# Kernel optimization log

Measured on AMD Instinct MI355X. Metric: run time of the kernel, lower is better.

Reference implementation:

```python
import jax, jax.numpy as jnp
import numpy as np

N_ITER = 2          # GenSP n_iter
M_COEF = 0.0        # GenSP M (grid strength)
AFF_SOFTMAX = 1.0   # GenSP affinity_softmax
NEG_INF = -1e30


def setup_inputs() -> dict:
    key = jax.random.key(0)
    x = jax.random.normal(key, (4, 64, 256, 256), dtype=jnp.float32)
    return {"x": x, "stoken": 16}


def _candidates(H, W, sh, sw, nH, nW):
    # 3x3 neighborhood of each pixel's initial superpixel (SSN / get_abs_indices)
    bi = jnp.arange(H) // sh
    bj = jnp.arange(W) // sw
    di = jnp.repeat(jnp.array([-1, 0, 1]), 3)   # (9,)
    dj = jnp.tile(jnp.array([-1, 0, 1]), 3)     # (9,)
    ci = bi[:, None, None] + di                 # (H,1,9)
    cj = bj[None, :, None] + dj                 # (1,W,9)
    valid = (ci >= 0) & (ci < nH) & (cj >= 0) & (cj < nW)        # (H,W,9)
    cand = jnp.clip(ci, 0, nH - 1) * nW + jnp.clip(cj, 0, nW - 1)  # (H,W,9)
    cand = jnp.broadcast_to(cand, (H, W, 9)).reshape(H * W, 9)
    valid = jnp.broadcast_to(valid, (H, W, 9)).reshape(H * W, 9)
    return cand, valid


def _affinity(feats, cent, cand, valid, nS):
    # feats: (B,Cf,P)  cent: (B,Cf,nS)  cand/valid: (P,9)
    B, Cf, P = feats.shape
    dot = jnp.einsum('bcp,bcs->bps', feats, cent)            # (B,P,nS) GEMM
    f2 = jnp.sum(feats * feats, axis=1)                      # (B,P)
    c2 = jnp.sum(cent * cent, axis=1)                        # (B,nS)
    dot9 = jnp.take_along_axis(dot, cand[None], axis=2)      # (B,P,9)
    dist = f2[..., None] + c2[:, cand] - 2.0 * dot9          # l2 distance (B,P,9)
    logits = jnp.where(valid[None], -AFF_SOFTMAX * dist, NEG_INF)
    aff9 = jax.nn.softmax(logits, axis=-1)                   # softmax_order 'v0'
    aff9 = jnp.where(valid[None], aff9, 0.0)
    # dense scatter: A[b, cand[p,k], p] += aff9[b,p,k]  -> (B,nS,P)
    pidx = jnp.arange(P)[:, None]
    A = jnp.zeros((B, nS, P), feats.dtype).at[:, cand, pidx].add(aff9)
    return A


def reference(x, stoken):
    B, C, H, W = x.shape
    sh = sw = int(stoken)
    nH, nW = (H - 1) // sh + 1, (W - 1) // sw + 1
    nS, P = nH * nW, H * W
    # append_grid: concat scaled pixel-coordinate channels (M / stoken)
    gi, gj = jnp.meshgrid(jnp.arange(H, dtype=x.dtype), jnp.arange(W, dtype=x.dtype), indexing='ij')
    grid = jnp.broadcast_to((M_COEF / sh) * jnp.stack([gi, gj]), (B, 2, H, W))
    feats = jnp.concatenate([x, grid], axis=1)               # (B,C+2,H,W)
    Cf = C + 2
    # init centroids: adaptive_avg_pool2d == block mean (H,W divisible by stoken)
    cent = feats.reshape(B, Cf, nH, sh, nW, sw).mean(axis=(3, 5)).reshape(B, Cf, nS)
    feats = feats.reshape(B, Cf, P)
    cand, valid = _candidates(H, W, sh, sw, nH, nW)
    A = None
    for k in range(N_ITER):
        A = _affinity(feats, cent, cand, valid, nS)          # (B,nS,P)
        if k < N_ITER - 1:
            num = jnp.einsum('bsp,bcp->bcs', A, feats)       # (B,Cf,nS)
            den = jnp.sum(A, axis=2)[:, None, :] + 1e-16
            cent = num / den
    return A
```

## Files before the change

kernel.cpp:

```cpp
#include <hip/hip_runtime.h>


#define PP 65536

typedef __attribute__((ext_vector_type(8))) short short8;
typedef __attribute__((ext_vector_type(4))) float f32x4;

__device__ __forceinline__ unsigned short f2bf(float f) {
  unsigned u = __float_as_uint(f);
  u += 0x7fff + ((u >> 16) & 1);
  return (unsigned short)(u >> 16);
}

__global__ __launch_bounds__(256) void k_init(const float* __restrict__ x,
                                              float* __restrict__ cent0,
                                              float4* __restrict__ zero4) {
  __shared__ float blk[64];
  int t = threadIdx.x;
  int wg = blockIdx.x;
  int cg = wg & 15, bi = (wg >> 4) & 15, b = wg >> 8;
  int tid = wg * 256 + t;
  if (tid < 16640) zero4[tid] = make_float4(0.f, 0.f, 0.f, 0.f);
  if (t < 64) blk[t] = 0.f;
  __syncthreads();
  int sub = t >> 6, j4 = t & 63;
#pragma unroll
  for (int q = 0; q < 4; q++) {
    int c = cg * 4 + q;
    const float4* xp4 =
        (const float4*)(x + ((long)(b * 64 + c) << 16) + ((bi * 16 + sub * 4) << 8)) + j4;
    float4 a = make_float4(0.f, 0.f, 0.f, 0.f);
#pragma unroll
    for (int r = 0; r < 4; r++) {
      float4 v = xp4[r * 64];
      a.x += v.x; a.y += v.y; a.z += v.z; a.w += v.w;
    }
    float ps = a.x + a.y + a.z + a.w;
    ps += __shfl_xor(ps, 1);
    ps += __shfl_xor(ps, 2);
    if ((j4 & 3) == 0) atomicAdd(&blk[(j4 >> 2) * 4 + q], ps);
  }
  __syncthreads();
  if (t < 64) {
    int sj = t >> 2, q = t & 3;
    cent0[(((b << 8) + bi * 16 + sj) << 6) + cg * 4 + q] = blk[t] * (1.f / 256.f);
  }
}

__global__ __launch_bounds__(256) void k_stat(const float* __restrict__ x,
                                              const float* __restrict__ cent,
                                              float* __restrict__ num,
                                              float* __restrict__ den) {
  __shared__ __align__(16) unsigned short xbf[64 * 264];
  __shared__ __align__(16) unsigned short affbf[16 * 264];
  __shared__ float cent_s[9 * 64];
  __shared__ float c2p[72];
  __shared__ float c2_s[9];
  __shared__ float den_s[36];
  __shared__ int scand[9];

  int t = threadIdx.x;
  int wg = blockIdx.x;
  int bj = wg & 15, bi = (wg >> 4) & 15, b = wg >> 8;

  if (t < 9) {
    int di = t / 3 - 1, dj = t % 3 - 1;
    int ci = bi + di, cj = bj + dj;
    int sc = min(max(ci, 0), 15) * 16 + min(max(cj, 0), 15);
    bool valid = ((unsigned)ci < 16u) && ((unsigned)cj < 16u);
    scand[t] = valid ? sc : (-1 - sc);
  }
  for (int o = t; o < 144; o += 256) {
    int k = o >> 4, f4 = o & 15;
    int di = k / 3 - 1, dj = k % 3 - 1;
    int sc = min(max(bi + di, 0), 15) * 16 + min(max(bj + dj, 0), 15);
    *(float4*)&cent_s[k * 64 + f4 * 4] =
        *(const float4*)(cent + (((b << 8) + sc) << 6) + f4 * 4);
  }
  __syncthreads();
  if (t < 72) {
    int k = t >> 3, pt = t & 7;
    float s = 0.f;
#pragma unroll
    for (int m = 0; m < 8; m++) { float v = cent_s[k * 64 + pt * 8 + m]; s += v * v; }
    c2p[t] = s;
  }
  __syncthreads();
  if (t < 9) {
    float s = 0.f;
#pragma unroll
    for (int m = 0; m < 8; m++) s += c2p[t * 8 + m];
    c2_s[t] = s;
  }
  __syncthreads();

  int vbits = 0;
#pragma unroll
  for (int k = 0; k < 9; k++) {
    int ci = bi + k / 3 - 1, cj = bj + k % 3 - 1;
    if ((unsigned)ci < 16u && (unsigned)cj < 16u) vbits |= 1 << k;
  }

  int r = t >> 4, col = t & 15;
  const float* base = x + ((long)(b * 64) << 16) + ((bi * 16 + r) << 8) + (bj * 16 + col);
  float acc[9];
#pragma unroll
  for (int k = 0; k < 9; k++) acc[k] = 0.f;
#pragma unroll 8
  for (int c = 0; c < 64; c++) {
    float xv = base[(long)c << 16];
    xbf[c * 264 + t] = f2bf(xv);
#pragma unroll
    for (int k = 0; k < 9; k++) acc[k] = fmaf(xv, cent_s[k * 64 + c], acc[k]);
  }
  float mx = -1e30f;
#pragma unroll
  for (int k = 0; k < 9; k++) {
    float l = 2.f * acc[k] - c2_s[k];
    acc[k] = ((vbits >> k) & 1) ? l : -1e30f;
    mx = fmaxf(mx, acc[k]);
  }
  float sum = 0.f;
#pragma unroll
  for (int k = 0; k < 9; k++) {
    acc[k] = __expf(acc[k] - mx);
    sum += acc[k];
  }
  float rs = 1.f / sum;
#pragma unroll
  for (int k = 0; k < 9; k++) {
    acc[k] *= rs;
    affbf[k * 264 + t] = f2bf(acc[k]);
  }

  int lane = t & 63, w = t >> 6;
#pragma unroll
  for (int k = 0; k < 9; k++) {
    float v = acc[k];
    v += __shfl_xor(v, 1);
    v += __shfl_xor(v, 2);
    v += __shfl_xor(v, 4);
    v += __shfl_xor(v, 8);
    v += __shfl_xor(v, 16);
    v += __shfl_xor(v, 32);
    if (lane == 0) den_s[w * 9 + k] = v;
  }
  __syncthreads();
  if (t < 9) {
    float d = den_s[t] + den_s[9 + t] + den_s[18 + t] + den_s[27 + t];
    int sc = scand[t]; sc = sc >= 0 ? sc : (-1 - sc);
    atomicAdd(&den[(b << 8) + sc], d);
  }

  int mrow = lane & 15;
  int quad = lane >> 4;
  f32x4 dacc = {0.f, 0.f, 0.f, 0.f};
#pragma unroll
  for (int ks = 0; ks < 8; ks++) {
    int p0 = ks * 32 + quad * 8;
    short8 a = *(const short8*)&xbf[(w * 16 + mrow) * 264 + p0];
    short8 bf = *(const short8*)&affbf[mrow * 264 + p0];
    dacc = __builtin_amdgcn_mfma_f32_16x16x32_bf16(a, bf, dacc, 0, 0, 0);
  }
  int kcol = lane & 15;
  if (kcol < 9) {
    int sc = scand[kcol]; sc = sc >= 0 ? sc : (-1 - sc);
    float* np = num + (((b << 8) + sc) << 6) + w * 16 + quad * 4;
    atomicAdd(&np[0], dacc[0]);
    atomicAdd(&np[1], dacc[1]);
    atomicAdd(&np[2], dacc[2]);
    atomicAdd(&np[3], dacc[3]);
  }
}

__global__ __launch_bounds__(256) void k_out(const float* __restrict__ x,
                                             const float* __restrict__ num,
                                             const float* __restrict__ den,
                                             f32x4* __restrict__ out4) {
  __shared__ float cent_s[48 * 68];
  __shared__ float den_s[48];
  __shared__ float c2p[384];
  __shared__ float c2_s[48];
  __shared__ float aff_t[9 * 260];

  int t = threadIdx.x;
  int wg = blockIdx.x;
  int h = wg & 1, i = (wg >> 1) & 255, b = wg >> 9;
  int bi = i >> 4;

  if (t < 48) {
    int ci = min(max(bi - 1 + (t >> 4), 0), 15);
    int cj = t & 15;
    den_s[t] = den[(b << 8) + ci * 16 + cj] + 1e-16f;
  }
  __syncthreads();
  for (int o = t; o < 768; o += 256) {
    int lr = o >> 4, f4i = o & 15;
    int ci = min(max(bi - 1 + (lr >> 4), 0), 15);
    int cj = lr & 15;
    float4 v = *(const float4*)(num + (((b << 8) + ci * 16 + cj) << 6) + f4i * 4);
    float inv = 1.f / den_s[lr];
    v.x *= inv; v.y *= inv; v.z *= inv; v.w *= inv;
    *(float4*)&cent_s[lr * 68 + f4i * 4] = v;
  }
  __syncthreads();
  for (int o = t; o < 384; o += 256) {
    int lr = o >> 3, pt = o & 7;
    float s = 0.f;
#pragma unroll
    for (int m = 0; m < 8; m++) { float v = cent_s[lr * 68 + pt * 8 + m]; s += v * v; }
    c2p[o] = s;
  }
  __syncthreads();
  if (t < 48) {
    float s = 0.f;
#pragma unroll
    for (int m = 0; m < 8; m++) s += c2p[t * 8 + m];
    c2_s[t] = s;
  }
  __syncthreads();

  int j = t, bj = j >> 4;
  int cidx[9];
  float c2k[9];
  int vbits = 0;
#pragma unroll
  for (int k = 0; k < 9; k++) {
    int di = k / 3 - 1, dj = k % 3 - 1;
    int ciu = bi + di, cju = bj + dj;
    if ((unsigned)ciu < 16u && (unsigned)cju < 16u) vbits |= 1 << k;
    int lidx = (di + 1) * 16 + min(max(cju, 0), 15);
    cidx[k] = lidx * 68;
    c2k[k] = c2_s[lidx];
  }
  const float* base = x + ((long)(b * 64) << 16) + (i << 8) + j;
  float acc[9];
#pragma unroll
  for (int k = 0; k < 9; k++) acc[k] = 0.f;
#pragma unroll 8
  for (int c = 0; c < 64; c++) {
    float xv = base[(long)c << 16];
#pragma unroll
    for (int k = 0; k < 9; k++) acc[k] = fmaf(xv, cent_s[cidx[k] + c], acc[k]);
  }
  float mx = -1e30f;
#pragma unroll
  for (int k = 0; k < 9; k++) {
    float l = 2.f * acc[k] - c2k[k];
    acc[k] = ((vbits >> k) & 1) ? l : -1e30f;
    mx = fmaxf(mx, acc[k]);
  }
  float sum = 0.f;
#pragma unroll
  for (int k = 0; k < 9; k++) {
    acc[k] = __expf(acc[k] - mx);
    sum += acc[k];
  }
  float rs = 1.f / sum;
#pragma unroll
  for (int k = 0; k < 9; k++) aff_t[k * 260 + j] = acc[k] * rs;
  __syncthreads();

  f32x4* obase = out4 + ((long)(b << 8) << 14) + (i << 6) + (t & 63);
  int j4 = t & 63;
  int w = t >> 6;
  int s0 = h << 7;
#pragma unroll 4
  for (int m = 0; m < 32; m++) {
    int s = s0 | (m << 2) | w;
    f32x4 v = {0.f, 0.f, 0.f, 0.f};
    int di = (s >> 4) - bi;
    if ((unsigned)(di + 1) <= 2u) {
      int dj = (s & 15) - (j4 >> 2);
      if ((unsigned)(dj + 1) <= 2u) {
        int k = (di + 1) * 3 + dj + 1;
        v = *(const f32x4*)&aff_t[k * 260 + (j4 << 2)];
      }
    }
    __builtin_nontemporal_store(v, &obase[(long)s << 14]);
  }
}

extern "C" void kernel_launch(void* const* d_in, const int* in_sizes, int n_in,
                              void* d_out, int out_size, void* d_ws, size_t ws_size,
                              hipStream_t stream) {
  const float* x = (const float*)d_in[0];
  float* out = (float*)d_out;
  float* ws = (float*)d_ws;

  float* num   = ws;
  float* den   = ws + 65536;
  float* cent0 = ws + 66560;

  k_init<<<1024, 256, 0, stream>>>(x, cent0, (float4*)ws);
  k_stat<<<1024, 256, 0, stream>>>(x, cent0, num, den);
  k_out<<<2048, 256, 0, stream>>>(x, num, den, (f32x4*)out);
}
```

Measured before the change: 353.0 us.

## Split final output stage into centroid, affinity, and dense-write kernels

```diff
diff --git a/kernel.cpp b/kernel.cpp
--- a/kernel.cpp
+++ b/kernel.cpp
@@ -170,6 +170,111 @@
     atomicAdd(&np[1], dacc[1]);
     atomicAdd(&np[2], dacc[2]);
     atomicAdd(&np[3], dacc[3]);
+  }
+}
+
+__global__ __launch_bounds__(256) void k_cent(const float* __restrict__ num,
+                                              const float* __restrict__ den,
+                                              float* __restrict__ cent1,
+                                              float* __restrict__ c2) {
+  int t = threadIdx.x;
+  int idx = blockIdx.x * 4 + (t >> 6);
+  int c = t & 63;
+  float d = den[idx] + 1e-16f;
+  float v = num[(idx << 6) + c] / d;
+  cent1[(idx << 6) + c] = v;
+  float s2 = v * v;
+  s2 += __shfl_xor(s2, 1);
+  s2 += __shfl_xor(s2, 2);
+  s2 += __shfl_xor(s2, 4);
+  s2 += __shfl_xor(s2, 8);
+  s2 += __shfl_xor(s2, 16);
+  s2 += __shfl_xor(s2, 32);
+  if (c == 0) c2[idx] = s2;
+}
+
+__global__ __launch_bounds__(256) void k_aff(const float* __restrict__ x,
+                                             const float* __restrict__ cent,
+                                             const float* __restrict__ c2,
+                                             float* __restrict__ aff) {
+  __shared__ float cent_s[9 * 64];
+  __shared__ float c2_s[9];
+
+  int t = threadIdx.x;
+  int wg = blockIdx.x;
+  int bj = wg & 15, bi = (wg >> 4) & 15, b = wg >> 8;
+
+  for (int o = t; o < 144; o += 256) {
+    int k = o >> 4, f4 = o & 15;
+    int sc = min(max(bi + k / 3 - 1, 0), 15) * 16 + min(max(bj + k % 3 - 1, 0), 15);
+    *(float4*)&cent_s[k * 64 + f4 * 4] =
+        *(const float4*)(cent + (((b << 8) + sc) << 6) + f4 * 4);
+  }
+  if (t < 9) {
+    int sc = min(max(bi + t / 3 - 1, 0), 15) * 16 + min(max(bj + t % 3 - 1, 0), 15);
+    c2_s[t] = c2[(b << 8) + sc];
+  }
+  __syncthreads();
+
+  int vbits = 0;
+#pragma unroll
+  for (int k = 0; k < 9; k++) {
+    int ci = bi + k / 3 - 1, cj = bj + k % 3 - 1;
+    if ((unsigned)ci < 16u && (unsigned)cj < 16u) vbits |= 1 << k;
+  }
+
+  int r = t >> 4, col = t & 15;
+  const float* base = x + ((long)(b * 64) << 16) + ((bi * 16 + r) << 8) + (bj * 16 + col);
+  float acc[9];
+#pragma unroll
+  for (int k = 0; k < 9; k++) acc[k] = 0.f;
+#pragma unroll 8
+  for (int c = 0; c < 64; c++) {
+    float xv = base[(long)c << 16];
+#pragma unroll
+    for (int k = 0; k < 9; k++) acc[k] = fmaf(xv, cent_s[k * 64 + c], acc[k]);
+  }
+  float mx = -1e30f;
+#pragma unroll
+  for (int k = 0; k < 9; k++) {
+    float l = 2.f * acc[k] - c2_s[k];
+    acc[k] = ((vbits >> k) & 1) ? l : -1e30f;
+    mx = fmaxf(mx, acc[k]);
+  }
+  float sum = 0.f;
+#pragma unroll
+  for (int k = 0; k < 9; k++) {
+    acc[k] = __expf(acc[k] - mx);
+    sum += acc[k];
+  }
+  float rs = 1.f / sum;
+  int p = ((bi * 16 + r) << 8) + (bj * 16 + col);
+#pragma unroll
+  for (int k = 0; k < 9; k++)
+    aff[(((long)(b * 9 + k)) << 16) + p] = acc[k] * rs;
+}
+
+__global__ __launch_bounds__(256) void k_write(const float* __restrict__ aff,
+                                               f32x4* __restrict__ out4) {
+  int t = threadIdx.x;
+  int wg = blockIdx.x;
+  int s = wg & 255, b = wg >> 8;
+  int si = s >> 4, sj = s & 15;
+  f32x4* op = out4 + ((long)wg << 14);
+  const f32x4 zero = {0.f, 0.f, 0.f, 0.f};
+#pragma unroll 4
+  for (int m = 0; m < 64; m++) {
+    int idx = m * 256 + t;
+    int i = idx >> 6, j4 = idx & 63;
+    int kr = si - (i >> 4) + 1;
+    int kc = sj - (j4 >> 2) + 1;
+    f32x4 v = zero;
+    if ((unsigned)kr <= 2u && (unsigned)kc <= 2u) {
+      int k = kr * 3 + kc;
+      const f32x4* ap = (const f32x4*)(aff + (((long)(b * 9 + k)) << 16));
+      v = ap[idx];
+    }
+    __builtin_nontemporal_store(v, &op[idx]);
   }
 }
 
@@ -291,8 +396,19 @@
   float* num   = ws;
   float* den   = ws + 65536;
   float* cent0 = ws + 66560;
+  float* cent1 = ws + 132096;
+  float* c2    = ws + 197632;
+  float* aff   = ws + 198656;
+  const size_t need_floats = 198656 + (size_t)4 * 9 * 65536;
 
   k_init<<<1024, 256, 0, stream>>>(x, cent0, (float4*)ws);
   k_stat<<<1024, 256, 0, stream>>>(x, cent0, num, den);
-  k_out<<<2048, 256, 0, stream>>>(x, num, den, (f32x4*)out);
-}
+
+  if (ws_size >= need_floats * sizeof(float)) {
+    k_cent<<<256, 256, 0, stream>>>(num, den, cent1, c2);
+    k_aff<<<1024, 256, 0, stream>>>(x, cent1, c2, aff);
+    k_write<<<1024, 256, 0, stream>>>(aff, (f32x4*)out);
+  } else {
+    k_out<<<2048, 256, 0, stream>>>(x, num, den, (f32x4*)out);
+  }
+}
```

New measurement: 373.1 us. 1.06x slower.

## Split affinity computation from dense output write into separate kernels

Applied to the files above, without the earlier changes.

```diff
diff --git a/kernel.cpp b/kernel.cpp
--- a/kernel.cpp
+++ b/kernel.cpp
@@ -173,46 +173,36 @@
   }
 }
 
-__global__ __launch_bounds__(256) void k_out(const float* __restrict__ x,
+__global__ __launch_bounds__(256) void k_aff(const float* __restrict__ x,
                                              const float* __restrict__ num,
                                              const float* __restrict__ den,
-                                             f32x4* __restrict__ out4) {
-  __shared__ float cent_s[48 * 68];
-  __shared__ float den_s[48];
-  __shared__ float c2p[384];
-  __shared__ float c2_s[48];
-  __shared__ float aff_t[9 * 260];
-
-  int t = threadIdx.x;
-  int wg = blockIdx.x;
-  int h = wg & 1, i = (wg >> 1) & 255, b = wg >> 9;
-  int bi = i >> 4;
-
-  if (t < 48) {
-    int ci = min(max(bi - 1 + (t >> 4), 0), 15);
-    int cj = t & 15;
-    den_s[t] = den[(b << 8) + ci * 16 + cj] + 1e-16f;
-  }
-  __syncthreads();
-  for (int o = t; o < 768; o += 256) {
-    int lr = o >> 4, f4i = o & 15;
-    int ci = min(max(bi - 1 + (lr >> 4), 0), 15);
-    int cj = lr & 15;
-    float4 v = *(const float4*)(num + (((b << 8) + ci * 16 + cj) << 6) + f4i * 4);
-    float inv = 1.f / den_s[lr];
+                                             float* __restrict__ aff) {
+  __shared__ float cent_s[9 * 64];
+  __shared__ float c2p[72];
+  __shared__ float c2_s[9];
+
+  int t = threadIdx.x;
+  int wg = blockIdx.x;
+  int bj = wg & 15, bi = (wg >> 4) & 15, b = wg >> 8;
+
+  if (t < 144) {
+    int k = t >> 4, f4 = t & 15;
+    int sc = min(max(bi + k / 3 - 1, 0), 15) * 16 + min(max(bj + k % 3 - 1, 0), 15);
+    float4 v = *(const float4*)(num + (((b << 8) + sc) << 6) + f4 * 4);
+    float inv = 1.f / (den[(b << 8) + sc] + 1e-16f);
     v.x *= inv; v.y *= inv; v.z *= inv; v.w *= inv;
-    *(float4*)&cent_s[lr * 68 + f4i * 4] = v;
-  }
-  __syncthreads();
-  for (int o = t; o < 384; o += 256) {
-    int lr = o >> 3, pt = o & 7;
-    float s = 0.f;
-#pragma unroll
-    for (int m = 0; m < 8; m++) { float v = cent_s[lr * 68 + pt * 8 + m]; s += v * v; }
-    c2p[o] = s;
-  }
-  __syncthreads();
-  if (t < 48) {
+    *(float4*)&cent_s[k * 64 + f4 * 4] = v;
+  }
+  __syncthreads();
+  if (t < 72) {
+    int k = t >> 3, pt = t & 7;
+    float s = 0.f;
+#pragma unroll
+    for (int m = 0; m < 8; m++) { float v = cent_s[k * 64 + pt * 8 + m]; s += v * v; }
+    c2p[t] = s;
+  }
+  __syncthreads();
+  if (t < 9) {
     float s = 0.f;
 #pragma unroll
     for (int m = 0; m < 8; m++) s += c2p[t * 8 + m];
@@ -220,20 +210,15 @@
   }
   __syncthreads();
 
-  int j = t, bj = j >> 4;
-  int cidx[9];
-  float c2k[9];
   int vbits = 0;
 #pragma unroll
   for (int k = 0; k < 9; k++) {
-    int di = k / 3 - 1, dj = k % 3 - 1;
-    int ciu = bi + di, cju = bj + dj;
-    if ((unsigned)ciu < 16u && (unsigned)cju < 16u) vbits |= 1 << k;
-    int lidx = (di + 1) * 16 + min(max(cju, 0), 15);
-    cidx[k] = lidx * 68;
-    c2k[k] = c2_s[lidx];
-  }
-  const float* base = x + ((long)(b * 64) << 16) + (i << 8) + j;
+    int ci = bi + k / 3 - 1, cj = bj + k % 3 - 1;
+    if ((unsigned)ci < 16u && (unsigned)cj < 16u) vbits |= 1 << k;
+  }
+
+  int r = t >> 4, col = t & 15;
+  const float* base = x + ((long)(b * 64) << 16) + ((bi * 16 + r) << 8) + (bj * 16 + col);
   float acc[9];
 #pragma unroll
   for (int k = 0; k < 9; k++) acc[k] = 0.f;
@@ -241,12 +226,12 @@
   for (int c = 0; c < 64; c++) {
     float xv = base[(long)c << 16];
 #pragma unroll
-    for (int k = 0; k < 9; k++) acc[k] = fmaf(xv, cent_s[cidx[k] + c], acc[k]);
+    for (int k = 0; k < 9; k++) acc[k] = fmaf(xv, cent_s[k * 64 + c], acc[k]);
   }
   float mx = -1e30f;
 #pragma unroll
   for (int k = 0; k < 9; k++) {
-    float l = 2.f * acc[k] - c2k[k];
+    float l = 2.f * acc[k] - c2_s[k];
     acc[k] = ((vbits >> k) & 1) ? l : -1e30f;
     mx = fmaxf(mx, acc[k]);
   }
@@ -257,27 +242,33 @@
     sum += acc[k];
   }
   float rs = 1.f / sum;
-#pragma unroll
-  for (int k = 0; k < 9; k++) aff_t[k * 260 + j] = acc[k] * rs;
-  __syncthreads();
-
-  f32x4* obase = out4 + ((long)(b << 8) << 14) + (i << 6) + (t & 63);
-  int j4 = t & 63;
-  int w = t >> 6;
-  int s0 = h << 7;
+  int p = ((bi * 16 + r) << 8) + (bj * 16 + col);
+#pragma unroll
+  for (int k = 0; k < 9; k++)
+    aff[(((long)(b * 9 + k)) << 16) + p] = acc[k] * rs;
+}
+
+__global__ __launch_bounds__(256) void k_write(const float* __restrict__ aff,
+                                               f32x4* __restrict__ out4) {
+  int t = threadIdx.x;
+  int wg = blockIdx.x;
+  int s = wg & 255, b = wg >> 8;
+  int si = s >> 4, sj = s & 15;
+  f32x4* op = out4 + ((long)wg << 14);
+  const f32x4 zero = {0.f, 0.f, 0.f, 0.f};
 #pragma unroll 4
-  for (int m = 0; m < 32; m++) {
-    int s = s0 | (m << 2) | w;
-    f32x4 v = {0.f, 0.f, 0.f, 0.f};
-    int di = (s >> 4) - bi;
-    if ((unsigned)(di + 1) <= 2u) {
-      int dj = (s & 15) - (j4 >> 2);
-      if ((unsigned)(dj + 1) <= 2u) {
-        int k = (di + 1) * 3 + dj + 1;
-        v = *(const f32x4*)&aff_t[k * 260 + (j4 << 2)];
-      }
+  for (int m = 0; m < 64; m++) {
+    int idx = m * 256 + t;
+    int i = idx >> 6, j4 = idx & 63;
+    int kr = si - (i >> 4) + 1;
+    int kc = sj - (j4 >> 2) + 1;
+    f32x4 v = zero;
+    if ((unsigned)kr <= 2u && (unsigned)kc <= 2u) {
+      int k = kr * 3 + kc;
+      const f32x4* ap = (const f32x4*)(aff + (((long)(b * 9 + k)) << 16));
+      v = ap[idx];
     }
-    __builtin_nontemporal_store(v, &obase[(long)s << 14]);
+    op[idx] = v;
   }
 }
 
@@ -291,8 +282,10 @@
   float* num   = ws;
   float* den   = ws + 65536;
   float* cent0 = ws + 66560;
+  float* aff   = ws + 132096;
 
   k_init<<<1024, 256, 0, stream>>>(x, cent0, (float4*)ws);
   k_stat<<<1024, 256, 0, stream>>>(x, cent0, num, den);
-  k_out<<<2048, 256, 0, stream>>>(x, num, den, (f32x4*)out);
-}
+  k_aff<<<1024, 256, 0, stream>>>(x, num, den, aff);
+  k_write<<<1024, 256, 0, stream>>>(aff, (f32x4*)out);
+}
```

Result: slower. 380.8 us (+7.9%).

## Fuse init, stat and output kernels into one cooperative kernel with grid barriers

Applied to the files above, without the earlier changes.

```diff
diff --git a/kernel.cpp b/kernel.cpp
--- a/kernel.cpp
+++ b/kernel.cpp
@@ -1,7 +1,5 @@
 #include <hip/hip_runtime.h>
 
-
-#define PP 65536
 
 typedef __attribute__((ext_vector_type(8))) short short8;
 typedef __attribute__((ext_vector_type(4))) float f32x4;
@@ -10,6 +8,311 @@
   unsigned u = __float_as_uint(f);
   u += 0x7fff + ((u >> 16) & 1);
   return (unsigned short)(u >> 16);
+}
+
+__device__ __forceinline__ void gridbar(int* ctr, int nblk) {
+  __syncthreads();
+  if (threadIdx.x == 0) {
+    __threadfence();
+    atomicAdd(ctr, 1);
+    int spins = 0;
+    while (__hip_atomic_load(ctr, __ATOMIC_ACQUIRE, __HIP_MEMORY_SCOPE_AGENT) < nblk) {
+      __builtin_amdgcn_s_sleep(8);
+      if (++spins > (1 << 20)) break;
+    }
+  }
+  __syncthreads();
+  __threadfence();
+}
+
+__global__ void k_zero(int* bar) {
+  if (threadIdx.x < 2) bar[threadIdx.x] = 0;
+}
+
+__global__ __launch_bounds__(256, 4) void k_fused(const float* __restrict__ x,
+                                                  float* __restrict__ ws,
+                                                  float* __restrict__ out,
+                                                  int* bar) {
+  __shared__ __align__(16) char smem[24336];
+  float* num = ws;
+  float* den = ws + 65536;
+  float* cent0 = ws + 66560;
+
+  int t = threadIdx.x;
+  int wg = blockIdx.x;
+
+  {
+    float* blk = (float*)smem;
+    int cg = wg & 15, bi = (wg >> 4) & 15, b = wg >> 8;
+    int tid = wg * 256 + t;
+    if (tid < 16640) ((float4*)ws)[tid] = make_float4(0.f, 0.f, 0.f, 0.f);
+    if (t < 64) blk[t] = 0.f;
+    __syncthreads();
+    int sub = t >> 6, j4 = t & 63;
+#pragma unroll
+    for (int q = 0; q < 4; q++) {
+      int c = cg * 4 + q;
+      const float4* xp4 =
+          (const float4*)(x + ((long)(b * 64 + c) << 16) + ((bi * 16 + sub * 4) << 8)) + j4;
+      float4 a = make_float4(0.f, 0.f, 0.f, 0.f);
+#pragma unroll
+      for (int r = 0; r < 4; r++) {
+        float4 v = xp4[r * 64];
+        a.x += v.x; a.y += v.y; a.z += v.z; a.w += v.w;
+      }
+      float ps = a.x + a.y + a.z + a.w;
+      ps += __shfl_xor(ps, 1);
+      ps += __shfl_xor(ps, 2);
+      if ((j4 & 3) == 0) atomicAdd(&blk[(j4 >> 2) * 4 + q], ps);
+    }
+    __syncthreads();
+    if (t < 64) {
+      int sj2 = t >> 2, q = t & 3;
+      cent0[(((b << 8) + bi * 16 + sj2) << 6) + cg * 4 + q] = blk[t] * (1.f / 256.f);
+    }
+  }
+
+  gridbar(bar + 0, (int)gridDim.x);
+
+  {
+    unsigned short* affbf = (unsigned short*)smem;
+    float* cent_s = (float*)(smem + 8448);
+    float* c2p = (float*)(smem + 10752);
+    float* c2_s = (float*)(smem + 11040);
+    float* den_s = (float*)(smem + 11076);
+    int* scand = (int*)(smem + 11220);
+
+    int bj = wg & 15, bi = (wg >> 4) & 15, b = wg >> 8;
+
+    if (t < 9) {
+      int di = t / 3 - 1, dj = t % 3 - 1;
+      int ci = bi + di, cj = bj + dj;
+      int sc = min(max(ci, 0), 15) * 16 + min(max(cj, 0), 15);
+      bool valid = ((unsigned)ci < 16u) && ((unsigned)cj < 16u);
+      scand[t] = valid ? sc : (-1 - sc);
+    }
+    if (t < 144) {
+      int k = t >> 4, f4 = t & 15;
+      int di = k / 3 - 1, dj = k % 3 - 1;
+      int sc = min(max(bi + di, 0), 15) * 16 + min(max(bj + dj, 0), 15);
+      *(float4*)&cent_s[k * 64 + f4 * 4] =
+          *(const float4*)(cent0 + (((b << 8) + sc) << 6) + f4 * 4);
+    }
+    __syncthreads();
+    if (t < 72) {
+      int k = t >> 3, pt = t & 7;
+      float s = 0.f;
+#pragma unroll
+      for (int m = 0; m < 8; m++) { float v = cent_s[k * 64 + pt * 8 + m]; s += v * v; }
+      c2p[t] = s;
+    }
+    __syncthreads();
+    if (t < 9) {
+      float s = 0.f;
+#pragma unroll
+      for (int m = 0; m < 8; m++) s += c2p[t * 8 + m];
+      c2_s[t] = s;
+    }
+    __syncthreads();
+
+    int vbits = 0;
+#pragma unroll
+    for (int k = 0; k < 9; k++) {
+      int ci = bi + k / 3 - 1, cj = bj + k % 3 - 1;
+      if ((unsigned)ci < 16u && (unsigned)cj < 16u) vbits |= 1 << k;
+    }
+
+    int lane = t & 63, w = t >> 6;
+    int mrow = lane & 15, quad = lane >> 4;
+
+    short8 areg[8];
+    {
+      int c = w * 16 + mrow;
+      const float* xrow = x + ((long)(b * 64 + c) << 16) + bi * 4096 +
+                          (quad >> 1) * 256 + bj * 16 + ((quad & 1) << 3);
+#pragma unroll
+      for (int ks = 0; ks < 8; ks++) {
+        float4 lo = *(const float4*)(xrow + ks * 512);
+        float4 hi = *(const float4*)(xrow + ks * 512 + 4);
+        short8 a;
+        a[0] = (short)f2bf(lo.x); a[1] = (short)f2bf(lo.y);
+        a[2] = (short)f2bf(lo.z); a[3] = (short)f2bf(lo.w);
+        a[4] = (short)f2bf(hi.x); a[5] = (short)f2bf(hi.y);
+        a[6] = (short)f2bf(hi.z); a[7] = (short)f2bf(hi.w);
+        areg[ks] = a;
+      }
+    }
+
+    int r = t >> 4, col = t & 15;
+    const float* base = x + ((long)(b * 64) << 16) + ((bi * 16 + r) << 8) + (bj * 16 + col);
+    float acc[9];
+#pragma unroll
+    for (int k = 0; k < 9; k++) acc[k] = 0.f;
+#pragma unroll 8
+    for (int c = 0; c < 64; c++) {
+      float xv = base[(long)c << 16];
+#pragma unroll
+      for (int k = 0; k < 9; k++) acc[k] = fmaf(xv, cent_s[k * 64 + c], acc[k]);
+    }
+    float mx = -1e30f;
+#pragma unroll
+    for (int k = 0; k < 9; k++) {
+      float l = 2.f * acc[k] - c2_s[k];
+      acc[k] = ((vbits >> k) & 1) ? l : -1e30f;
+      mx = fmaxf(mx, acc[k]);
+    }
+    float sum = 0.f;
+#pragma unroll
+    for (int k = 0; k < 9; k++) {
+      acc[k] = __expf(acc[k] - mx);
+      sum += acc[k];
+    }
+    float rs = 1.f / sum;
+#pragma unroll
+    for (int k = 0; k < 9; k++) {
+      acc[k] *= rs;
+      affbf[k * 264 + t] = f2bf(acc[k]);
+    }
+
+#pragma unroll
+    for (int k = 0; k < 9; k++) {
+      float v = acc[k];
+      v += __shfl_xor(v, 1);
+      v += __shfl_xor(v, 2);
+      v += __shfl_xor(v, 4);
+      v += __shfl_xor(v, 8);
+      v += __shfl_xor(v, 16);
+      v += __shfl_xor(v, 32);
+      if (lane == 0) den_s[w * 9 + k] = v;
+    }
+    __syncthreads();
+    if (t < 9) {
+      float d = den_s[t] + den_s[9 + t] + den_s[18 + t] + den_s[27 + t];
+      int sc = scand[t]; sc = sc >= 0 ? sc : (-1 - sc);
+      atomicAdd(&den[(b << 8) + sc], d);
+    }
+
+    f32x4 dacc = {0.f, 0.f, 0.f, 0.f};
+#pragma unroll
+    for (int ks = 0; ks < 8; ks++) {
+      int p0 = ks * 32 + quad * 8;
+      short8 bf = *(const short8*)&affbf[mrow * 264 + p0];
+      dacc = __builtin_amdgcn_mfma_f32_16x16x32_bf16(areg[ks], bf, dacc, 0, 0, 0);
+    }
+    int kcol = lane & 15;
+    if (kcol < 9) {
+      int sc = scand[kcol]; sc = sc >= 0 ? sc : (-1 - sc);
+      float* np = num + (((b << 8) + sc) << 6) + w * 16 + quad * 4;
+      atomicAdd(&np[0], dacc[0]);
+      atomicAdd(&np[1], dacc[1]);
+      atomicAdd(&np[2], dacc[2]);
+      atomicAdd(&np[3], dacc[3]);
+    }
+  }
+
+  gridbar(bar + 1, (int)gridDim.x);
+
+  {
+    float* cent_s = (float*)smem;
+    float* aff_t = (float*)(smem + 13056);
+    float* c2p = (float*)(smem + 22416);
+    float* den_s = (float*)(smem + 23952);
+    float* c2_s = (float*)(smem + 24144);
+
+    int i = wg & 255, b = wg >> 8;
+    int bi = i >> 4;
+
+    if (t < 48) {
+      int ci = min(max(bi - 1 + (t >> 4), 0), 15);
+      int cj = t & 15;
+      den_s[t] = den[(b << 8) + ci * 16 + cj] + 1e-16f;
+    }
+    __syncthreads();
+    for (int o = t; o < 768; o += 256) {
+      int lr = o >> 4, f4i = o & 15;
+      int ci = min(max(bi - 1 + (lr >> 4), 0), 15);
+      int cj = lr & 15;
+      float4 v = *(const float4*)(num + (((b << 8) + ci * 16 + cj) << 6) + f4i * 4);
+      float inv = 1.f / den_s[lr];
+      v.x *= inv; v.y *= inv; v.z *= inv; v.w *= inv;
+      *(float4*)&cent_s[lr * 68 + f4i * 4] = v;
+    }
+    __syncthreads();
+    for (int o = t; o < 384; o += 256) {
+      int lr = o >> 3, pt = o & 7;
+      float s = 0.f;
+#pragma unroll
+      for (int m = 0; m < 8; m++) { float v = cent_s[lr * 68 + pt * 8 + m]; s += v * v; }
+      c2p[o] = s;
+    }
+    __syncthreads();
+    if (t < 48) {
+      float s = 0.f;
+#pragma unroll
+      for (int m = 0; m < 8; m++) s += c2p[t * 8 + m];
+      c2_s[t] = s;
+    }
+    __syncthreads();
+
+    int j = t, bj = j >> 4;
+    int cidx[9];
+    float c2k[9];
+    int vbits = 0;
+#pragma unroll
+    for (int k = 0; k < 9; k++) {
+      int di = k / 3 - 1, dj = k % 3 - 1;
+      int ciu = bi + di, cju = bj + dj;
+      if ((unsigned)ciu < 16u && (unsigned)cju < 16u) vbits |= 1 << k;
+      int lidx = (di + 1) * 16 + min(max(cju, 0), 15);
+      cidx[k] = lidx * 68;
+      c2k[k] = c2_s[lidx];
+    }
+    const float* base = x + ((long)(b * 64) << 16) + (i << 8) + j;
+    float acc[9];
+#pragma unroll
+    for (int k = 0; k < 9; k++) acc[k] = 0.f;
+#pragma unroll 8
+    for (int c = 0; c < 64; c++) {
+      float xv = base[(long)c << 16];
+#pragma unroll
+      for (int k = 0; k < 9; k++) acc[k] = fmaf(xv, cent_s[cidx[k] + c], acc[k]);
+    }
+    float mx = -1e30f;
+#pragma unroll
+    for (int k = 0; k < 9; k++) {
+      float l = 2.f * acc[k] - c2k[k];
+      acc[k] = ((vbits >> k) & 1) ? l : -1e30f;
+      mx = fmaxf(mx, acc[k]);
+    }
+    float sum = 0.f;
+#pragma unroll
+    for (int k = 0; k < 9; k++) {
+      acc[k] = __expf(acc[k] - mx);
+      sum += acc[k];
+    }
+    float rs = 1.f / sum;
+#pragma unroll
+    for (int k = 0; k < 9; k++) aff_t[k * 260 + j] = acc[k] * rs;
+    __syncthreads();
+
+    f32x4* obase = (f32x4*)out + ((long)(b << 8) << 14) + (i << 6) + (t & 63);
+    int j4 = t & 63;
+    int w2 = t >> 6;
+#pragma unroll 4
+    for (int m = 0; m < 64; m++) {
+      int s = (m << 2) | w2;
+      f32x4 v = {0.f, 0.f, 0.f, 0.f};
+      int di = (s >> 4) - bi;
+      if ((unsigned)(di + 1) <= 2u) {
+        int dj = (s & 15) - (j4 >> 2);
+        if ((unsigned)(dj + 1) <= 2u) {
+          int k = (di + 1) * 3 + dj + 1;
+          v = *(const f32x4*)&aff_t[k * 260 + (j4 << 2)];
+        }
+      }
+      __builtin_nontemporal_store(v, &obase[(long)s << 14]);
+    }
+  }
 }
 
 __global__ __launch_bounds__(256) void k_init(const float* __restrict__ x,
@@ -291,8 +594,17 @@
   float* num   = ws;
   float* den   = ws + 65536;
   float* cent0 = ws + 66560;
-
-  k_init<<<1024, 256, 0, stream>>>(x, cent0, (float4*)ws);
-  k_stat<<<1024, 256, 0, stream>>>(x, cent0, num, den);
-  k_out<<<2048, 256, 0, stream>>>(x, num, den, (f32x4*)out);
-}
+  int* bar     = (int*)(ws + 132096);
+
+  k_zero<<<1, 64, 0, stream>>>(bar);
+
+  void* args[] = {(void*)&x, (void*)&ws, (void*)&out, (void*)&bar};
+  hipError_t e = hipLaunchCooperativeKernel((const void*)k_fused, dim3(1024),
+                                            dim3(256), args, 0, stream);
+  if (e != hipSuccess) {
+    (void)hipGetLastError();
+    k_init<<<1024, 256, 0, stream>>>(x, cent0, (float4*)ws);
+    k_stat<<<1024, 256, 0, stream>>>(x, cent0, num, den);
+    k_out<<<2048, 256, 0, stream>>>(x, num, den, (f32x4*)out);
+  }
+}
```

Measured after the change: 778.1 us. 120% more time.
